# Kernel tuning notes

Hardware: AMD Instinct MI355X
Metric: run time of the kernel (lower is better)

## Reference

```python
import jax, jax.numpy as jnp
import numpy as np

# Module constants (from init_kwargs)
NB_IN = 4          # num_blocks_in
NB_OUT = 8         # num_blocks_out
BS_IN = 128        # block_size_in (hard-coded in source)
NHID = 4096
BS_OUT = NHID // NB_OUT   # 512, also att_out
TOPK = 4
DK = 64            # d_k = d_v, n_head = 1


def _group_linear(x, w):
    # x: (B, n_blocks, d_in), w: (n_blocks, d_in, d_out) -> (B, n_blocks, d_out)
    return jnp.einsum('bnd,nde->bne', x, w)


def _attend(q, k, v):
    # single-head scaled dot-product attention
    attn = jax.nn.softmax(jnp.einsum('bqd,bkd->bqk', q, k) / jnp.sqrt(jnp.asarray(DK, q.dtype)), axis=-1)
    return jnp.einsum('bqk,bkd->bqd', attn, v), attn


def setup_inputs() -> dict:
    key = jax.random.key(0)
    ks = jax.random.split(key, 20)
    s = 0.02
    d = {
        'inp': jax.random.normal(ks[0], (1024, NB_IN * BS_IN), jnp.float32),
        'hx': jax.random.normal(ks[1], (1024, NHID), jnp.float32),
        'cx': jax.random.normal(ks[2], (1024, NHID), jnp.float32),
        # inp_att (residual=False): GroupLinear q/k/v + fc
        'ia_wq': jax.random.normal(ks[3], (NB_OUT, BS_OUT, DK), jnp.float32) * s,
        'ia_wk': jax.random.normal(ks[4], (NB_IN + 1, BS_IN, DK), jnp.float32) * s,
        'ia_wv': jax.random.normal(ks[5], (NB_IN + 1, BS_IN, DK), jnp.float32) * s,
        'ia_fc_w': jax.random.normal(ks[6], (DK, BS_OUT), jnp.float32) * s,
        'ia_fc_b': jnp.zeros((BS_OUT,), jnp.float32),
        # mha (residual=True, gated)
        'mha_wq': jax.random.normal(ks[7], (NB_OUT, BS_OUT, DK), jnp.float32) * s,
        'mha_wk': jax.random.normal(ks[8], (NB_OUT, BS_OUT, DK), jnp.float32) * s,
        'mha_wv': jax.random.normal(ks[9], (NB_OUT, BS_OUT, DK), jnp.float32) * s,
        'mha_fc_w': jax.random.normal(ks[10], (DK, BS_OUT), jnp.float32) * s,
        'mha_fc_b': jnp.zeros((BS_OUT,), jnp.float32),
        'mha_gate_w': jax.random.normal(ks[11], (DK, BS_OUT), jnp.float32) * s,
        'mha_gate_b': jnp.zeros((BS_OUT,), jnp.float32),
        # block-diagonal LSTM (BlockLSTM after blockify_params): per-block LSTMCell
        'w_ih': jax.random.normal(ks[12], (NB_OUT, BS_OUT, 4 * BS_OUT), jnp.float32) * s,
        'w_hh': jax.random.normal(ks[13], (NB_OUT, BS_OUT, 4 * BS_OUT), jnp.float32) * s,
        'b_ih': jnp.zeros((NB_OUT, 4 * BS_OUT), jnp.float32),
        'b_hh': jnp.zeros((NB_OUT, 4 * BS_OUT), jnp.float32),
    }
    return d


def _forward(inp, hx, cx, ia_wq, ia_wk, ia_wv, ia_fc_w, ia_fc_b,
             mha_wq, mha_wk, mha_wv, mha_fc_w, mha_fc_b, mha_gate_w, mha_gate_b,
             w_ih, w_hh, b_ih, b_hh):
    B = inp.shape[0]
    # --- input attention (inp_att) ---
    x = inp.reshape(B, NB_IN, BS_IN)
    x = jnp.concatenate([x, jnp.zeros_like(x[:, :1])], axis=1)        # append null block -> (B, NB_IN+1, BS_IN)
    hb = hx.reshape(B, NB_OUT, BS_OUT)
    q = _group_linear(hb, ia_wq)                                      # (B, NB_OUT, DK)
    k = _group_linear(x, ia_wk)
    v = _group_linear(x, ia_wv)
    o, iatt = _attend(q, k, v)                                        # o:(B,NB_OUT,DK), iatt:(B,NB_OUT,NB_IN+1)
    inp_use = (o @ ia_fc_w + ia_fc_b).reshape(B, NB_OUT * BS_OUT)     # residual=False path

    # --- top-k block selection mask (detached) ---
    score = iatt[:, :, 0]                                             # (B, NB_OUT)
    thr = jax.lax.top_k(score, TOPK)[0][:, -1]                        # k-th largest per sample
    mask_blk = (score > thr[:, None] - 0.01).astype(hx.dtype)         # (B, NB_OUT)
    mask = jnp.broadcast_to(mask_blk[:, :, None], (B, NB_OUT, BS_OUT)).reshape(B, NHID)
    mask = jax.lax.stop_gradient(mask)

    # --- block-diagonal LSTM update ---
    xb = inp_use.reshape(B, NB_OUT, BS_OUT)
    cb = cx.reshape(B, NB_OUT, BS_OUT)
    gates = (jnp.einsum('bkd,kdg->bkg', xb, w_ih) + b_ih
             + jnp.einsum('bkd,kdg->bkg', hb, w_hh) + b_hh)           # (B, NB_OUT, 4*BS_OUT)
    i_g, f_g, g_g, o_g = jnp.split(gates, 4, axis=-1)
    c_new = jax.nn.sigmoid(f_g) * cb + jax.nn.sigmoid(i_g) * jnp.tanh(g_g)
    h_new = jax.nn.sigmoid(o_g) * jnp.tanh(c_new)                     # (B, NB_OUT, BS_OUT)
    cx_new = c_new.reshape(B, NHID)

    # --- inter-block attention (step_att, residual + gate) ---
    residual = h_new
    q2 = _group_linear(h_new, mha_wq)
    k2 = _group_linear(h_new, mha_wk)
    v2 = _group_linear(h_new, mha_wv)
    o2, _ = _attend(q2, k2, v2)                                       # (B, NB_OUT, DK)
    out = o2 @ mha_fc_w + mha_fc_b
    gate = jax.nn.sigmoid(o2 @ mha_gate_w + mha_gate_b)
    hx_new = (residual + gate * jnp.tanh(out)).reshape(B, NHID)

    # --- masked blend of old / new states ---
    hx_out = mask * hx_new + (1.0 - mask) * hx
    cx_out = mask * cx_new + (1.0 - mask) * cx
    return hx_out, cx_out, mask


def reference(inp, hx, cx, ia_wq, ia_wk, ia_wv, ia_fc_w, ia_fc_b,
              mha_wq, mha_wk, mha_wv, mha_fc_w, mha_fc_b, mha_gate_w, mha_gate_b,
              w_ih, w_hh, b_ih, b_hh):
    return _forward(inp, hx, cx, ia_wq, ia_wk, ia_wv, ia_fc_w, ia_fc_b,
                    mha_wq, mha_wk, mha_wv, mha_fc_w, mha_fc_b, mha_gate_w, mha_gate_b,
                    w_ih, w_hh, b_ih, b_hh)
```

## Files before the change

### kernel.cpp

```cpp
#include <hip/hip_runtime.h>
#include <hip/hip_bf16.h>

#define B_    1024
#define NHID_ 4096
#define NBO   8
#define BSO   512
#define DK_   64

typedef __bf16 bf16;
typedef __bf16 bf16x2 __attribute__((ext_vector_type(2)));
typedef __bf16 bf16x4 __attribute__((ext_vector_type(4)));
typedef __bf16 bf16x8 __attribute__((ext_vector_type(8)));
typedef float  f32x4  __attribute__((ext_vector_type(4)));

__device__ __forceinline__ float sigf(float x){ return 1.0f/(1.0f + __expf(-x)); }

__device__ __forceinline__ void gload16(const void* g, void* lds){
    __builtin_amdgcn_global_load_lds((const __attribute__((address_space(1))) unsigned int*)g,
                                     (__attribute__((address_space(3))) unsigned int*)lds,
                                     16, 0, 0);
}

__global__ __launch_bounds__(256) void k_prep(
    const float* __restrict__ hx,
    const float* __restrict__ mha_wq, const float* __restrict__ mha_wk,
    const float* __restrict__ mha_wv, const float* __restrict__ ia_fc_w,
    const float* __restrict__ fc_w, const float* __restrict__ gate_w,
    bf16* __restrict__ hb16, bf16* __restrict__ wqkvT,
    bf16* __restrict__ iafcT, bf16* __restrict__ fcgT)
{
    int gid = blockIdx.x*256 + threadIdx.x;
    if (gid < 1048576){
        float4 v = ((const float4*)hx)[gid];
        bf16x4 o; o.x=(bf16)v.x; o.y=(bf16)v.y; o.z=(bf16)v.z; o.w=(bf16)v.w;
        *(bf16x4*)&hb16[(size_t)gid*4] = o;
        return;
    }
    int e = gid - 1048576;
    if (e < 786432){
        int col = e >> 9, k = e & 511;
        int n = col / 192, c = col - n*192;
        int p = c >> 6, ee = c & 63;
        const float* s = (p==0) ? mha_wq : ((p==1) ? mha_wk : mha_wv);
        wqkvT[e] = (bf16)s[((size_t)n*512 + k)*64 + ee];
        return;
    }
    e -= 786432;
    if (e < 32768){
        int c = e>>6, k = e&63;
        iafcT[e] = (bf16)ia_fc_w[(size_t)k*512 + c];
        return;
    }
    e -= 32768;
    if (e < 65536){
        int cg = e>>6, k = e&63;
        int ct = cg>>6, j = cg&63;
        const float* s = (j<32) ? fc_w : gate_w;
        int col = ct*32 + (j&31);
        fcgT[e] = (bf16)s[(size_t)k*512 + col];
    }
}

__global__ __launch_bounds__(256) void k_wtrans(const float* __restrict__ w_ih,
                                                const float* __restrict__ w_hh,
                                                bf16* __restrict__ wT)
{
    int n = blockIdx.z >> 1, which = blockIdx.z & 1;
    int k0 = blockIdx.y * 64, c0 = blockIdx.x * 64;
    const float* src = (which ? w_hh : w_ih) + (size_t)n*512*2048;
    __shared__ float tile[64][65];
    int t = threadIdx.x;
    #pragma unroll
    for (int it=0; it<4; ++it){
        int idx = t + it*256;
        int r = idx>>4, c4 = (idx&15)*4;
        *(float4*)&tile[r][c4] = *(const float4*)&src[(size_t)(k0+r)*2048 + c0 + c4];
    }
    __syncthreads();
    #pragma unroll
    for (int it=0; it<2; ++it){
        int idx = t + it*256;
        int c = idx>>3, r8 = (idx&7)*8;
        bf16x8 v;
        #pragma unroll
        for (int jj=0;jj<8;++jj) v[jj] = (bf16)tile[r8+jj][c];
        *(bf16x8*)&wT[((size_t)n*2048 + c0 + c)*1024 + which*512 + k0 + r8] = v;
    }
}

__global__ __launch_bounds__(256) void k_qkv(const float* __restrict__ hx,
                                             const float* __restrict__ inp,
                                             const float* __restrict__ ia_wq,
                                             const float* __restrict__ ia_wk,
                                             const float* __restrict__ ia_wv,
                                             float* __restrict__ qbuf,
                                             float* __restrict__ kbuf,
                                             float* __restrict__ vbuf)
{
    int b0 = blockIdx.x*64, y = blockIdx.y, t = threadIdx.x;
    int tx = t&15, ty = t>>4;
    __shared__ float A_s[64][20];
    __shared__ float W1_s[16][68];
    __shared__ float W2_s[16][68];
    if (y < 8){
        int n = y;
        float acc[4][4] = {};
        for (int k0=0; k0<512; k0+=16){
            { int row=t>>2, seg=(t&3)*4;
              *(float4*)&A_s[row][seg] = *(const float4*)&hx[(size_t)(b0+row)*4096 + n*512 + k0 + seg]; }
            { int kk=t>>4, e4=(t&15)*4;
              *(float4*)&W1_s[kk][e4] = *(const float4*)&ia_wq[(size_t)n*32768 + (size_t)(k0+kk)*64 + e4]; }
            __syncthreads();
            #pragma unroll
            for (int kk=0; kk<16; ++kk){
                float4 wv = *(float4*)&W1_s[kk][tx*4];
                #pragma unroll
                for (int r=0;r<4;++r){
                    float a = A_s[ty*4+r][kk];
                    acc[r][0]+=a*wv.x; acc[r][1]+=a*wv.y; acc[r][2]+=a*wv.z; acc[r][3]+=a*wv.w;
                }
            }
            __syncthreads();
        }
        #pragma unroll
        for (int r=0;r<4;++r){
            float4 o; o.x=acc[r][0]; o.y=acc[r][1]; o.z=acc[r][2]; o.w=acc[r][3];
            *(float4*)&qbuf[(size_t)(b0+ty*4+r)*512 + n*64 + tx*4] = o;
        }
    } else {
        int j = y-8;
        float ak[4][4] = {}, av[4][4] = {};
        for (int k0=0; k0<128; k0+=16){
            { int row=t>>2, seg=(t&3)*4;
              *(float4*)&A_s[row][seg] = *(const float4*)&inp[(size_t)(b0+row)*512 + j*128 + k0 + seg]; }
            { int kk=t>>4, e4=(t&15)*4;
              *(float4*)&W1_s[kk][e4] = *(const float4*)&ia_wk[(size_t)j*8192 + (size_t)(k0+kk)*64 + e4];
              *(float4*)&W2_s[kk][e4] = *(const float4*)&ia_wv[(size_t)j*8192 + (size_t)(k0+kk)*64 + e4]; }
            __syncthreads();
            #pragma unroll
            for (int kk=0; kk<16; ++kk){
                float4 wk = *(float4*)&W1_s[kk][tx*4];
                float4 wv = *(float4*)&W2_s[kk][tx*4];
                #pragma unroll
                for (int r=0;r<4;++r){
                    float a = A_s[ty*4+r][kk];
                    ak[r][0]+=a*wk.x; ak[r][1]+=a*wk.y; ak[r][2]+=a*wk.z; ak[r][3]+=a*wk.w;
                    av[r][0]+=a*wv.x; av[r][1]+=a*wv.y; av[r][2]+=a*wv.z; av[r][3]+=a*wv.w;
                }
            }
            __syncthreads();
        }
        #pragma unroll
        for (int r=0;r<4;++r){
            float4 ok; ok.x=ak[r][0]; ok.y=ak[r][1]; ok.z=ak[r][2]; ok.w=ak[r][3];
            float4 ov; ov.x=av[r][0]; ov.y=av[r][1]; ov.z=av[r][2]; ov.w=av[r][3];
            *(float4*)&kbuf[(size_t)(b0+ty*4+r)*256 + j*64 + tx*4] = ok;
            *(float4*)&vbuf[(size_t)(b0+ty*4+r)*256 + j*64 + tx*4] = ov;
        }
    }
}

__global__ __launch_bounds__(256) void k_score(const float* __restrict__ qbuf,
                                               const float* __restrict__ kbuf,
                                               const float* __restrict__ vbuf,
                                               bf16* __restrict__ obuf,
                                               float* __restrict__ maskb,
                                               float* __restrict__ mask_out)
{
    int t = threadIdx.x, sb = t>>6, ts = t&63;
    int b = blockIdx.x*4 + sb;
    __shared__ float q_s[4][512];
    __shared__ float k_s[4][256];
    __shared__ float v_s[4][256];
    __shared__ float at_s[4][40];
    __shared__ float sc_s[4][8];
    __shared__ float mb_s[4][8];

    #pragma unroll
    for (int r=0;r<8;++r) q_s[sb][ts+r*64] = qbuf[(size_t)b*512 + ts + r*64];
    #pragma unroll
    for (int r=0;r<4;++r){
        k_s[sb][ts+r*64] = kbuf[(size_t)b*256 + ts + r*64];
        v_s[sb][ts+r*64] = vbuf[(size_t)b*256 + ts + r*64];
    }
    __syncthreads();
    if (ts < 40){
        int n = ts/5, j = ts%5;
        float s = 0.f;
        if (j < 4){
            const float* q = &q_s[sb][n*64];
            const float* k = &k_s[sb][j*64];
            for (int e=0;e<64;++e) s += q[e]*k[e];
            s *= 0.125f;
        }
        at_s[sb][ts] = s;
    }
    __syncthreads();
    if (ts < 8){
        float m = at_s[sb][ts*5];
        for (int j=1;j<5;++j) m = fmaxf(m, at_s[sb][ts*5+j]);
        float ex[5]; float sum=0.f;
        for (int j=0;j<5;++j){ ex[j]=__expf(at_s[sb][ts*5+j]-m); sum+=ex[j]; }
        float inv = 1.f/sum;
        for (int j=0;j<5;++j) at_s[sb][ts*5+j] = ex[j]*inv;
        sc_s[sb][ts] = ex[0]*inv;
    }
    __syncthreads();
    if (ts == 0){
        float s[8];
        for (int nn=0;nn<8;++nn) s[nn] = sc_s[sb][nn];
        for (int ii=1;ii<8;++ii){ float key=s[ii]; int jj=ii-1;
            while(jj>=0 && s[jj]<key){ s[jj+1]=s[jj]; --jj; } s[jj+1]=key; }
        float thr = s[3]-0.01f;
        for (int nn=0;nn<8;++nn) mb_s[sb][nn] = (sc_s[sb][nn] > thr) ? 1.0f : 0.0f;
    }
    __syncthreads();
    #pragma unroll
    for (int r=0;r<8;++r){
        int i = ts + r*64;
        int n = i>>6, e = i&63;
        float s = 0.f;
        #pragma unroll
        for (int j=0;j<4;++j) s += at_s[sb][n*5+j]*v_s[sb][j*64+e];
        obuf[(size_t)b*512 + i] = (bf16)s;
    }
    if (ts < 8) maskb[b*8+ts] = mb_s[sb][ts];
    float4* mo = (float4*)(mask_out + (size_t)b*4096);
    #pragma unroll
    for (int r=0;r<16;++r){
        int i4 = ts + r*64;
        float m = mb_s[sb][i4>>7];
        float4 mv; mv.x=m; mv.y=m; mv.z=m; mv.w=m;
        mo[i4] = mv;
    }
}

__global__ __launch_bounds__(256) void k_fc_ia(const bf16* __restrict__ obuf,
                                               const bf16* __restrict__ iafcT,
                                               const float* __restrict__ ia_fc_b,
                                               bf16* __restrict__ xb16)
{
    int bx = blockIdx.x, by = blockIdx.y;
    int t = threadIdx.x, w = t>>6, l = t&63, quad = l>>4, l16 = l&15;
    int wm = w&1, wd = w>>1;
    __shared__ bf16 A_s[64*72];
    __shared__ bf16 W_s[64*72];
    #pragma unroll
    for (int j=0;j<2;++j){
        int c = t + j*256;
        int row = c>>3, seg = c&7;
        *(bf16x8*)&A_s[row*72 + seg*8] = *(const bf16x8*)&obuf[((size_t)bx*64+row)*64 + seg*8];
        *(bf16x8*)&W_s[row*72 + seg*8] = *(const bf16x8*)&iafcT[((size_t)by*64+row)*64 + seg*8];
    }
    __syncthreads();
    f32x4 zero = {0.f,0.f,0.f,0.f};
    f32x4 acc[2][2] = {{zero,zero},{zero,zero}};
    #pragma unroll
    for (int k0=0;k0<64;k0+=32){
        bf16x8 a[2], bb[2];
        #pragma unroll
        for (int r=0;r<2;++r) a[r] = *(const bf16x8*)&A_s[(wm*32+r*16+l16)*72 + k0 + quad*8];
        #pragma unroll
        for (int c=0;c<2;++c) bb[c] = *(const bf16x8*)&W_s[(wd*32+c*16+l16)*72 + k0 + quad*8];
        #pragma unroll
        for (int r=0;r<2;++r)
            #pragma unroll
            for (int c=0;c<2;++c)
                acc[r][c] = __builtin_amdgcn_mfma_f32_16x16x32_bf16(a[r], bb[c], acc[r][c], 0,0,0);
    }
    #pragma unroll
    for (int c=0;c<2;++c){
        int col = by*64 + wd*32 + c*16 + l16;
        float bias = ia_fc_b[col];
        #pragma unroll
        for (int r=0;r<2;++r)
            #pragma unroll
            for (int v=0;v<4;++v){
                int row = bx*64 + wm*32 + r*16 + quad*4 + v;
                xb16[(size_t)row*512 + col] = (bf16)(acc[r][c][v] + bias);
            }
    }
}

__global__ __launch_bounds__(256,4) void k_lstm(
    const bf16* __restrict__ xb16, const bf16* __restrict__ hb16,
    const bf16* __restrict__ wT, const float* __restrict__ b_ih,
    const float* __restrict__ b_hh, const float* __restrict__ cx,
    const float* __restrict__ maskb,
    float* __restrict__ cx_out, bf16* __restrict__ hn16)
{
    int bid = blockIdx.x;
    int n = bid & 7;
    int i = bid >> 3;
    int d0 = (i & 15) * 32;
    int b0 = (i >> 4) * 128;
    int t = threadIdx.x;
    int w = t >> 6, l = t & 63;
    int quad = l >> 4, l16 = l & 15;
    int wm = w & 1, wd = w >> 1;

    __shared__ bf16 A_s[512*8];
    __shared__ bf16 W_s[512*8];

    f32x4 zero = {0.f,0.f,0.f,0.f};
    f32x4 acc[4][4];
    #pragma unroll
    for (int rf=0;rf<4;++rf)
        #pragma unroll
        for (int g=0;g<4;++g) acc[rf][g] = zero;

    const bf16* wbase = wT + (size_t)n*2048*1024;

    for (int k0 = 0; k0 < 1024; k0 += 32){
        const bf16* ab = (k0 < 512) ? (xb16 + (size_t)n*512 + k0)
                                    : (hb16 + (size_t)n*512 + (k0-512));
        #pragma unroll
        for (int j=0;j<2;++j){
            int slot = j*256 + w*64 + l;
            int row = slot>>2, ss = slot&3;
            int seg = ss ^ ((row>>1)&3);
            gload16(ab + (size_t)(b0+row)*4096 + seg*8, &A_s[(size_t)(j*256 + w*64)*8]);
        }
        #pragma unroll
        for (int j=0;j<2;++j){
            int slot = j*256 + w*64 + l;
            int col = slot>>2, ss = slot&3;
            int seg = ss ^ ((col>>1)&3);
            int g = col>>5, dl = col&31;
            gload16(wbase + (size_t)(g*512 + d0 + dl)*1024 + k0 + seg*8,
                    &W_s[(size_t)(j*256 + w*64)*8]);
        }
        __syncthreads();
        bf16x8 a[4];
        #pragma unroll
        for (int rf=0;rf<4;++rf){
            int row = wm*64 + rf*16 + l16;
            int slot = row*4 + (quad ^ ((row>>1)&3));
            a[rf] = *(const bf16x8*)&A_s[slot*8];
        }
        #pragma unroll
        for (int g=0; g<4; ++g){
            int col = g*32 + wd*16 + l16;
            int slot = col*4 + (quad ^ ((col>>1)&3));
            bf16x8 bb = *(const bf16x8*)&W_s[slot*8];
            #pragma unroll
            for (int rf=0;rf<4;++rf)
                acc[rf][g] = __builtin_amdgcn_mfma_f32_16x16x32_bf16(a[rf], bb, acc[rf][g], 0,0,0);
        }
        __syncthreads();
    }

    int d = d0 + wd*16 + l16;
    float bi  = b_ih[n*2048 +        d] + b_hh[n*2048 +        d];
    float bff = b_ih[n*2048 +  512 + d] + b_hh[n*2048 +  512 + d];
    float bg  = b_ih[n*2048 + 1024 + d] + b_hh[n*2048 + 1024 + d];
    float bo  = b_ih[n*2048 + 1536 + d] + b_hh[n*2048 + 1536 + d];
    #pragma unroll
    for (int rf=0;rf<4;++rf){
        #pragma unroll
        for (int v=0;v<4;++v){
            int row = b0 + wm*64 + rf*16 + quad*4 + v;
            float gi = acc[rf][0][v] + bi;
            float gf = acc[rf][1][v] + bff;
            float gg = acc[rf][2][v] + bg;
            float go = acc[rf][3][v] + bo;
            size_t gidx = (size_t)row*4096 + n*512 + d;
            float cb = cx[gidx];
            float cn = sigf(gf)*cb + sigf(gi)*tanhf(gg);
            float hn = sigf(go)*tanhf(cn);
            float m  = maskb[row*8+n];
            cx_out[gidx] = (m != 0.f) ? cn : cb;
            hn16[gidx]   = (bf16)hn;
        }
    }
}

__global__ __launch_bounds__(256) void k_proj64(const bf16* __restrict__ hn16,
                                                const bf16* __restrict__ wqkvT,
                                                float* __restrict__ qkv2)
{
    int b0 = blockIdx.x*64, n = blockIdx.y, ct = blockIdx.z;
    int t = threadIdx.x, w = t>>6, l = t&63, quad = l>>4, l16 = l&15;
    int wm = w&1, wd = w>>1;
    __shared__ bf16 A_s[256*8];
    __shared__ bf16 B_s[256*8];
    f32x4 zero = {0.f,0.f,0.f,0.f};
    f32x4 acc[2][2] = {{zero,zero},{zero,zero}};
    const bf16* ab = hn16 + (size_t)n*512;
    const bf16* wb = wqkvT + ((size_t)n*192 + ct*64)*512;

    for (int k0=0;k0<512;k0+=32){
        {
            int slot = t;
            int row = slot>>2, ss = slot&3;
            int seg = ss ^ ((row>>1)&3);
            gload16(ab + (size_t)(b0+row)*4096 + k0 + seg*8, &A_s[(size_t)(w*64)*8]);
            gload16(wb + (size_t)row*512      + k0 + seg*8, &B_s[(size_t)(w*64)*8]);
        }
        __syncthreads();
        bf16x8 a[2], bb[2];
        #pragma unroll
        for (int r=0;r<2;++r){
            int row = wm*32 + r*16 + l16;
            int slot = row*4 + (quad ^ ((row>>1)&3));
            a[r] = *(const bf16x8*)&A_s[slot*8];
        }
        #pragma unroll
        for (int c=0;c<2;++c){
            int col = wd*32 + c*16 + l16;
            int slot = col*4 + (quad ^ ((col>>1)&3));
            bb[c] = *(const bf16x8*)&B_s[slot*8];
        }
        #pragma unroll
        for (int r=0;r<2;++r)
            #pragma unroll
            for (int c=0;c<2;++c)
                acc[r][c] = __builtin_amdgcn_mfma_f32_16x16x32_bf16(a[r], bb[c], acc[r][c], 0,0,0);
        __syncthreads();
    }
    #pragma unroll
    for (int c=0;c<2;++c){
        int col = ct*64 + wd*32 + c*16 + l16;
        #pragma unroll
        for (int r=0;r<2;++r)
            #pragma unroll
            for (int v=0;v<4;++v){
                int row = b0 + wm*32 + r*16 + quad*4 + v;
                qkv2[(size_t)row*1536 + n*192 + col] = acc[r][c][v];
            }
    }
}

__global__ __launch_bounds__(256) void k_att2(const float* __restrict__ qkv2,
                                              bf16* __restrict__ o2buf)
{
    int t = threadIdx.x, sb = t>>6, ts = t&63;
    int b = blockIdx.x*4 + sb;
    __shared__ float q_s[4][512];
    __shared__ float k_s[4][512];
    __shared__ float v_s[4][512];
    __shared__ float at_s[4][64];
    #pragma unroll
    for (int r=0;r<8;++r){
        int i = ts + r*64;
        int n = i>>6, e = i&63;
        const float* src = qkv2 + (size_t)b*1536 + n*192;
        q_s[sb][i] = src[e];
        k_s[sb][i] = src[64+e];
        v_s[sb][i] = src[128+e];
    }
    __syncthreads();
    {
        int n = ts>>3, j = ts&7;
        float s = 0.f;
        const float* q = &q_s[sb][n*64];
        const float* k = &k_s[sb][j*64];
        for (int e=0;e<64;++e) s += q[e]*k[e];
        at_s[sb][ts] = s*0.125f;
    }
    __syncthreads();
    if (ts < 8){
        float m = at_s[sb][ts*8];
        for (int j=1;j<8;++j) m = fmaxf(m, at_s[sb][ts*8+j]);
        float ex[8]; float sum=0.f;
        for (int j=0;j<8;++j){ ex[j]=__expf(at_s[sb][ts*8+j]-m); sum+=ex[j]; }
        float inv = 1.f/sum;
        for (int j=0;j<8;++j) at_s[sb][ts*8+j] = ex[j]*inv;
    }
    __syncthreads();
    #pragma unroll
    for (int r=0;r<8;++r){
        int i = ts + r*64;
        int n = i>>6, e = i&63;
        float s = 0.f;
        #pragma unroll
        for (int j=0;j<8;++j) s += at_s[sb][n*8+j]*v_s[sb][j*64+e];
        o2buf[(size_t)b*512 + i] = (bf16)s;
    }
}

__global__ __launch_bounds__(256) void k_fcgate(const bf16* __restrict__ o2buf,
                                                const bf16* __restrict__ fcgT,
                                                const float* __restrict__ fc_b,
                                                const float* __restrict__ gate_b,
                                                const bf16* __restrict__ hn16,
                                                const float* __restrict__ hx,
                                                const float* __restrict__ maskb,
                                                float* __restrict__ hx_out)
{
    int bx = blockIdx.x, ct = blockIdx.y;
    int t = threadIdx.x, w = t>>6, l = t&63, quad = l>>4, l16 = l&15;
    __shared__ bf16 A_s[64*72];
    __shared__ bf16 W_s[64*72];
    #pragma unroll
    for (int j=0;j<2;++j){
        int c = t + j*256;
        int row = c>>3, seg = c&7;
        *(bf16x8*)&A_s[row*72 + seg*8] = *(const bf16x8*)&o2buf[((size_t)bx*64+row)*64 + seg*8];
        *(bf16x8*)&W_s[row*72 + seg*8] = *(const bf16x8*)&fcgT[((size_t)ct*64+row)*64 + seg*8];
    }
    __syncthreads();
    f32x4 zero = {0.f,0.f,0.f,0.f};
    f32x4 acc[4] = {zero,zero,zero,zero};
    #pragma unroll
    for (int k0=0;k0<64;k0+=32){
        bf16x8 a = *(const bf16x8*)&A_s[(w*16+l16)*72 + k0 + quad*8];
        #pragma unroll
        for (int c=0;c<4;++c){
            bf16x8 bb = *(const bf16x8*)&W_s[(c*16+l16)*72 + k0 + quad*8];
            acc[c] = __builtin_amdgcn_mfma_f32_16x16x32_bf16(a, bb, acc[c], 0,0,0);
        }
    }
    #pragma unroll
    for (int c=0;c<2;++c){
        int d = ct*32 + c*16 + l16;
        float fb = fc_b[d], gb = gate_b[d];
        #pragma unroll
        for (int v=0;v<4;++v){
            int row = bx*64 + w*16 + quad*4 + v;
            int b = row>>3, n = row&7;
            size_t idx = (size_t)b*4096 + n*512 + d;
            float f = acc[c][v]   + fb;
            float g = acc[c+2][v] + gb;
            float hn = (float)hn16[idx];
            float m = maskb[row];
            hx_out[idx] = (m != 0.f) ? (hn + sigf(g)*tanhf(f)) : hx[idx];
        }
    }
}

extern "C" void kernel_launch(void* const* d_in, const int* in_sizes, int n_in,
                              void* d_out, int out_size, void* d_ws, size_t ws_size,
                              hipStream_t stream)
{
    const float* inp       = (const float*)d_in[0];
    const float* hx        = (const float*)d_in[1];
    const float* cx        = (const float*)d_in[2];
    const float* ia_wq     = (const float*)d_in[3];
    const float* ia_wk     = (const float*)d_in[4];
    const float* ia_wv     = (const float*)d_in[5];
    const float* ia_fc_w   = (const float*)d_in[6];
    const float* ia_fc_b   = (const float*)d_in[7];
    const float* mha_wq    = (const float*)d_in[8];
    const float* mha_wk    = (const float*)d_in[9];
    const float* mha_wv    = (const float*)d_in[10];
    const float* mha_fc_w  = (const float*)d_in[11];
    const float* mha_fc_b  = (const float*)d_in[12];
    const float* mha_gate_w= (const float*)d_in[13];
    const float* mha_gate_b= (const float*)d_in[14];
    const float* w_ih      = (const float*)d_in[15];
    const float* w_hh      = (const float*)d_in[16];
    const float* b_ih      = (const float*)d_in[17];
    const float* b_hh      = (const float*)d_in[18];

    float* hx_out  = (float*)d_out;
    float* cx_out  = hx_out + (size_t)B_*NHID_;
    float* mask_out= cx_out + (size_t)B_*NHID_;

    char* p = (char*)d_ws;
    bf16* wT     = (bf16*)p;               p += (size_t)8*2048*1024*2;
    bf16* hb16   = (bf16*)p;               p += (size_t)B_*NHID_*2;
    bf16* xb16   = (bf16*)p;               p += (size_t)B_*NHID_*2;
    bf16* hn16   = (bf16*)p;               p += (size_t)B_*NHID_*2;
    bf16* wqkvT  = (bf16*)p;               p += (size_t)8*192*512*2;
    bf16* iafcT  = (bf16*)p;               p += (size_t)512*64*2;
    bf16* fcgT   = (bf16*)p;               p += (size_t)1024*64*2;
    float* qbuf  = (float*)p;              p += (size_t)B_*512*4;
    float* kbuf  = (float*)p;              p += (size_t)B_*256*4;
    float* vbuf  = (float*)p;              p += (size_t)B_*256*4;
    bf16* obuf   = (bf16*)p;               p += (size_t)B_*8*64*2;
    bf16* o2buf  = (bf16*)p;               p += (size_t)B_*8*64*2;
    float* qkv2  = (float*)p;              p += (size_t)B_*1536*4;
    float* maskb = (float*)p;              p += (size_t)B_*8*4;

    hipLaunchKernelGGL(k_prep, dim3(7552), dim3(256), 0, stream,
                       hx, mha_wq, mha_wk, mha_wv, ia_fc_w, mha_fc_w, mha_gate_w,
                       hb16, wqkvT, iafcT, fcgT);
    hipLaunchKernelGGL(k_wtrans, dim3(32,8,16), dim3(256), 0, stream, w_ih, w_hh, wT);
    hipLaunchKernelGGL(k_qkv, dim3(16,12), dim3(256), 0, stream,
                       hx, inp, ia_wq, ia_wk, ia_wv, qbuf, kbuf, vbuf);
    hipLaunchKernelGGL(k_score, dim3(256), dim3(256), 0, stream,
                       qbuf, kbuf, vbuf, obuf, maskb, mask_out);
    hipLaunchKernelGGL(k_fc_ia, dim3(128,8), dim3(256), 0, stream, obuf, iafcT, ia_fc_b, xb16);
    hipLaunchKernelGGL(k_lstm, dim3(1024), dim3(256), 0, stream,
                       xb16, hb16, wT, b_ih, b_hh, cx, maskb, cx_out, hn16);
    hipLaunchKernelGGL(k_proj64, dim3(16,8,3), dim3(256), 0, stream, hn16, wqkvT, qkv2);
    hipLaunchKernelGGL(k_att2, dim3(256), dim3(256), 0, stream, qkv2, o2buf);
    hipLaunchKernelGGL(k_fcgate, dim3(128,16), dim3(256), 0, stream,
                       o2buf, fcgT, mha_fc_b, mha_gate_b, hn16, hx, maskb, hx_out);
}
```

Baseline: 317.7 us.

## Double-buffer LSTM and proj GEMMs, merge weight transpose into prep, retile qkv

Several independent changes ship together. The LSTM and proj64 GEMMs now double-buffer their LDS tiles, so the next K-slice's global_load_lds is issued before the current slice's MFMAs and one barrier per iteration is dropped. The w_ih/w_hh transpose kernel is folded into k_prep to save a launch. k_qkv uses 32-row tiles with a K step of 32 for more blocks, k_fcgate processes two column tiles per block, and sigmoid/tanh use a fast rcp-based approximation. These add LDS pressure and may cost a little accuracy in tanh.

```diff
diff --git a/kernel.cpp b/kernel.cpp
--- a/kernel.cpp
+++ b/kernel.cpp
@@ -13,7 +13,14 @@
 typedef __bf16 bf16x8 __attribute__((ext_vector_type(8)));
 typedef float  f32x4  __attribute__((ext_vector_type(4)));
 
-__device__ __forceinline__ float sigf(float x){ return 1.0f/(1.0f + __expf(-x)); }
+__device__ __forceinline__ float sigf(float x){
+    float e = __expf(-x);
+    return __builtin_amdgcn_rcpf(1.0f + e);
+}
+__device__ __forceinline__ float ftanh(float x){
+    float e = __expf(2.0f*x);
+    return 1.0f - 2.0f*__builtin_amdgcn_rcpf(e + 1.0f);
+}
 
 __device__ __forceinline__ void gload16(const void* g, void* lds){
     __builtin_amdgcn_global_load_lds((const __attribute__((address_space(1))) unsigned int*)g,
@@ -22,14 +29,42 @@
 }
 
 __global__ __launch_bounds__(256) void k_prep(
+    const float* __restrict__ w_ih, const float* __restrict__ w_hh,
     const float* __restrict__ hx,
     const float* __restrict__ mha_wq, const float* __restrict__ mha_wk,
     const float* __restrict__ mha_wv, const float* __restrict__ ia_fc_w,
     const float* __restrict__ fc_w, const float* __restrict__ gate_w,
-    bf16* __restrict__ hb16, bf16* __restrict__ wqkvT,
+    bf16* __restrict__ wT, bf16* __restrict__ hb16, bf16* __restrict__ wqkvT,
     bf16* __restrict__ iafcT, bf16* __restrict__ fcgT)
 {
-    int gid = blockIdx.x*256 + threadIdx.x;
+    int bid = blockIdx.x;
+    int t = threadIdx.x;
+    if (bid < 4096){
+        int c0 = (bid & 31)*64;
+        int k0 = ((bid>>5)&7)*64;
+        int z  = bid>>8;
+        int n = z>>1, which = z&1;
+        const float* src = (which ? w_hh : w_ih) + (size_t)n*512*2048;
+        __shared__ float tile[64][65];
+        #pragma unroll
+        for (int it=0; it<4; ++it){
+            int idx = t + it*256;
+            int r = idx>>4, c4 = (idx&15)*4;
+            *(float4*)&tile[r][c4] = *(const float4*)&src[(size_t)(k0+r)*2048 + c0 + c4];
+        }
+        __syncthreads();
+        #pragma unroll
+        for (int it=0; it<2; ++it){
+            int idx = t + it*256;
+            int c = idx>>3, r8 = (idx&7)*8;
+            bf16x8 v;
+            #pragma unroll
+            for (int jj=0;jj<8;++jj) v[jj] = (bf16)tile[r8+jj][c];
+            *(bf16x8*)&wT[((size_t)n*2048 + c0 + c)*1024 + which*512 + k0 + r8] = v;
+        }
+        return;
+    }
+    int gid = (bid-4096)*256 + t;
     if (gid < 1048576){
         float4 v = ((const float4*)hx)[gid];
         bf16x4 o; o.x=(bf16)v.x; o.y=(bf16)v.y; o.z=(bf16)v.z; o.w=(bf16)v.w;
@@ -61,33 +96,6 @@
     }
 }
 
-__global__ __launch_bounds__(256) void k_wtrans(const float* __restrict__ w_ih,
-                                                const float* __restrict__ w_hh,
-                                                bf16* __restrict__ wT)
-{
-    int n = blockIdx.z >> 1, which = blockIdx.z & 1;
-    int k0 = blockIdx.y * 64, c0 = blockIdx.x * 64;
-    const float* src = (which ? w_hh : w_ih) + (size_t)n*512*2048;
-    __shared__ float tile[64][65];
-    int t = threadIdx.x;
-    #pragma unroll
-    for (int it=0; it<4; ++it){
-        int idx = t + it*256;
-        int r = idx>>4, c4 = (idx&15)*4;
-        *(float4*)&tile[r][c4] = *(const float4*)&src[(size_t)(k0+r)*2048 + c0 + c4];
-    }
-    __syncthreads();
-    #pragma unroll
-    for (int it=0; it<2; ++it){
-        int idx = t + it*256;
-        int c = idx>>3, r8 = (idx&7)*8;
-        bf16x8 v;
-        #pragma unroll
-        for (int jj=0;jj<8;++jj) v[jj] = (bf16)tile[r8+jj][c];
-        *(bf16x8*)&wT[((size_t)n*2048 + c0 + c)*1024 + which*512 + k0 + r8] = v;
-    }
-}
-
 __global__ __launch_bounds__(256) void k_qkv(const float* __restrict__ hx,
                                              const float* __restrict__ inp,
                                              const float* __restrict__ ia_wq,
@@ -97,65 +105,82 @@
                                              float* __restrict__ kbuf,
                                              float* __restrict__ vbuf)
 {
-    int b0 = blockIdx.x*64, y = blockIdx.y, t = threadIdx.x;
+    int b0 = blockIdx.x*32, y = blockIdx.y, t = threadIdx.x;
     int tx = t&15, ty = t>>4;
-    __shared__ float A_s[64][20];
-    __shared__ float W1_s[16][68];
-    __shared__ float W2_s[16][68];
+    __shared__ float Af[32][36];
+    __shared__ float W1[32][68];
+    __shared__ float W2[32][68];
     if (y < 8){
         int n = y;
-        float acc[4][4] = {};
-        for (int k0=0; k0<512; k0+=16){
-            { int row=t>>2, seg=(t&3)*4;
-              *(float4*)&A_s[row][seg] = *(const float4*)&hx[(size_t)(b0+row)*4096 + n*512 + k0 + seg]; }
-            { int kk=t>>4, e4=(t&15)*4;
-              *(float4*)&W1_s[kk][e4] = *(const float4*)&ia_wq[(size_t)n*32768 + (size_t)(k0+kk)*64 + e4]; }
+        float acc[2][4] = {};
+        for (int k0=0; k0<512; k0+=32){
+            { int row=t>>3, c4=(t&7)*4;
+              *(float4*)&Af[row][c4] = *(const float4*)&hx[(size_t)(b0+row)*4096 + n*512 + k0 + c4]; }
+            #pragma unroll
+            for (int j=0;j<2;++j){
+                int id = j*256 + t;
+                int kk = id>>4, e4 = (id&15)*4;
+                *(float4*)&W1[kk][e4] = *(const float4*)&ia_wq[(size_t)n*32768 + (size_t)(k0+kk)*64 + e4];
+            }
             __syncthreads();
             #pragma unroll
-            for (int kk=0; kk<16; ++kk){
-                float4 wv = *(float4*)&W1_s[kk][tx*4];
+            for (int kk4=0; kk4<8; ++kk4){
+                float4 a0 = *(float4*)&Af[ty*2  ][kk4*4];
+                float4 a1 = *(float4*)&Af[ty*2+1][kk4*4];
                 #pragma unroll
-                for (int r=0;r<4;++r){
-                    float a = A_s[ty*4+r][kk];
-                    acc[r][0]+=a*wv.x; acc[r][1]+=a*wv.y; acc[r][2]+=a*wv.z; acc[r][3]+=a*wv.w;
+                for (int j=0;j<4;++j){
+                    float4 wv = *(float4*)&W1[kk4*4+j][tx*4];
+                    float s0 = (j==0)?a0.x:((j==1)?a0.y:((j==2)?a0.z:a0.w));
+                    float s1 = (j==0)?a1.x:((j==1)?a1.y:((j==2)?a1.z:a1.w));
+                    acc[0][0]+=s0*wv.x; acc[0][1]+=s0*wv.y; acc[0][2]+=s0*wv.z; acc[0][3]+=s0*wv.w;
+                    acc[1][0]+=s1*wv.x; acc[1][1]+=s1*wv.y; acc[1][2]+=s1*wv.z; acc[1][3]+=s1*wv.w;
                 }
             }
             __syncthreads();
         }
         #pragma unroll
-        for (int r=0;r<4;++r){
+        for (int r=0;r<2;++r){
             float4 o; o.x=acc[r][0]; o.y=acc[r][1]; o.z=acc[r][2]; o.w=acc[r][3];
-            *(float4*)&qbuf[(size_t)(b0+ty*4+r)*512 + n*64 + tx*4] = o;
+            *(float4*)&qbuf[(size_t)(b0+ty*2+r)*512 + n*64 + tx*4] = o;
         }
     } else {
-        int j = y-8;
-        float ak[4][4] = {}, av[4][4] = {};
-        for (int k0=0; k0<128; k0+=16){
-            { int row=t>>2, seg=(t&3)*4;
-              *(float4*)&A_s[row][seg] = *(const float4*)&inp[(size_t)(b0+row)*512 + j*128 + k0 + seg]; }
-            { int kk=t>>4, e4=(t&15)*4;
-              *(float4*)&W1_s[kk][e4] = *(const float4*)&ia_wk[(size_t)j*8192 + (size_t)(k0+kk)*64 + e4];
-              *(float4*)&W2_s[kk][e4] = *(const float4*)&ia_wv[(size_t)j*8192 + (size_t)(k0+kk)*64 + e4]; }
+        int jb = y-8;
+        float ak[2][4] = {}, av[2][4] = {};
+        for (int k0=0; k0<128; k0+=32){
+            { int row=t>>3, c4=(t&7)*4;
+              *(float4*)&Af[row][c4] = *(const float4*)&inp[(size_t)(b0+row)*512 + jb*128 + k0 + c4]; }
+            #pragma unroll
+            for (int j=0;j<2;++j){
+                int id = j*256 + t;
+                int kk = id>>4, e4 = (id&15)*4;
+                *(float4*)&W1[kk][e4] = *(const float4*)&ia_wk[(size_t)jb*8192 + (size_t)(k0+kk)*64 + e4];
+                *(float4*)&W2[kk][e4] = *(const float4*)&ia_wv[(size_t)jb*8192 + (size_t)(k0+kk)*64 + e4];
+            }
             __syncthreads();
             #pragma unroll
-            for (int kk=0; kk<16; ++kk){
-                float4 wk = *(float4*)&W1_s[kk][tx*4];
-                float4 wv = *(float4*)&W2_s[kk][tx*4];
+            for (int kk4=0; kk4<8; ++kk4){
+                float4 a0 = *(float4*)&Af[ty*2  ][kk4*4];
+                float4 a1 = *(float4*)&Af[ty*2+1][kk4*4];
                 #pragma unroll
-                for (int r=0;r<4;++r){
-                    float a = A_s[ty*4+r][kk];
-                    ak[r][0]+=a*wk.x; ak[r][1]+=a*wk.y; ak[r][2]+=a*wk.z; ak[r][3]+=a*wk.w;
-                    av[r][0]+=a*wv.x; av[r][1]+=a*wv.y; av[r][2]+=a*wv.z; av[r][3]+=a*wv.w;
+                for (int j=0;j<4;++j){
+                    float4 wk = *(float4*)&W1[kk4*4+j][tx*4];
+                    float4 wv = *(float4*)&W2[kk4*4+j][tx*4];
+                    float s0 = (j==0)?a0.x:((j==1)?a0.y:((j==2)?a0.z:a0.w));
+                    float s1 = (j==0)?a1.x:((j==1)?a1.y:((j==2)?a1.z:a1.w));
+                    ak[0][0]+=s0*wk.x; ak[0][1]+=s0*wk.y; ak[0][2]+=s0*wk.z; ak[0][3]+=s0*wk.w;
+                    ak[1][0]+=s1*wk.x; ak[1][1]+=s1*wk.y; ak[1][2]+=s1*wk.z; ak[1][3]+=s1*wk.w;
+                    av[0][0]+=s0*wv.x; av[0][1]+=s0*wv.y; av[0][2]+=s0*wv.z; av[0][3]+=s0*wv.w;
+                    av[1][0]+=s1*wv.x; av[1][1]+=s1*wv.y; av[1][2]+=s1*wv.z; av[1][3]+=s1*wv.w;
                 }
             }
             __syncthreads();
         }
         #pragma unroll
-        for (int r=0;r<4;++r){
+        for (int r=0;r<2;++r){
             float4 ok; ok.x=ak[r][0]; ok.y=ak[r][1]; ok.z=ak[r][2]; ok.w=ak[r][3];
             float4 ov; ov.x=av[r][0]; ov.y=av[r][1]; ov.z=av[r][2]; ov.w=av[r][3];
-            *(float4*)&kbuf[(size_t)(b0+ty*4+r)*256 + j*64 + tx*4] = ok;
-            *(float4*)&vbuf[(size_t)(b0+ty*4+r)*256 + j*64 + tx*4] = ov;
+            *(float4*)&kbuf[(size_t)(b0+ty*2+r)*256 + jb*64 + tx*4] = ok;
+            *(float4*)&vbuf[(size_t)(b0+ty*2+r)*256 + jb*64 + tx*4] = ov;
         }
     }
 }
@@ -299,8 +324,8 @@
     int quad = l >> 4, l16 = l & 15;
     int wm = w & 1, wd = w >> 1;
 
-    __shared__ bf16 A_s[512*8];
-    __shared__ bf16 W_s[512*8];
+    __shared__ bf16 A_s[2][512*8];
+    __shared__ bf16 W_s[2][512*8];
 
     f32x4 zero = {0.f,0.f,0.f,0.f};
     f32x4 acc[4][4];
@@ -311,7 +336,7 @@
 
     const bf16* wbase = wT + (size_t)n*2048*1024;
 
-    for (int k0 = 0; k0 < 1024; k0 += 32){
+    auto stage = [&](int buf, int k0){
         const bf16* ab = (k0 < 512) ? (xb16 + (size_t)n*512 + k0)
                                     : (hb16 + (size_t)n*512 + (k0-512));
         #pragma unroll
@@ -319,7 +344,7 @@
             int slot = j*256 + w*64 + l;
             int row = slot>>2, ss = slot&3;
             int seg = ss ^ ((row>>1)&3);
-            gload16(ab + (size_t)(b0+row)*4096 + seg*8, &A_s[(size_t)(j*256 + w*64)*8]);
+            gload16(ab + (size_t)(b0+row)*4096 + seg*8, &A_s[buf][(j*256 + w*64)*8]);
         }
         #pragma unroll
         for (int j=0;j<2;++j){
@@ -328,26 +353,31 @@
             int seg = ss ^ ((col>>1)&3);
             int g = col>>5, dl = col&31;
             gload16(wbase + (size_t)(g*512 + d0 + dl)*1024 + k0 + seg*8,
-                    &W_s[(size_t)(j*256 + w*64)*8]);
-        }
+                    &W_s[buf][(j*256 + w*64)*8]);
+        }
+    };
+
+    stage(0, 0);
+    for (int it = 0; it < 32; ++it){
         __syncthreads();
+        if (it < 31) stage((it+1)&1, (it+1)*32);
+        int buf = it & 1;
         bf16x8 a[4];
         #pragma unroll
         for (int rf=0;rf<4;++rf){
             int row = wm*64 + rf*16 + l16;
             int slot = row*4 + (quad ^ ((row>>1)&3));
-            a[rf] = *(const bf16x8*)&A_s[slot*8];
+            a[rf] = *(const bf16x8*)&A_s[buf][slot*8];
         }
         #pragma unroll
         for (int g=0; g<4; ++g){
             int col = g*32 + wd*16 + l16;
             int slot = col*4 + (quad ^ ((col>>1)&3));
-            bf16x8 bb = *(const bf16x8*)&W_s[slot*8];
+            bf16x8 bb = *(const bf16x8*)&W_s[buf][slot*8];
             #pragma unroll
             for (int rf=0;rf<4;++rf)
                 acc[rf][g] = __builtin_amdgcn_mfma_f32_16x16x32_bf16(a[rf], bb, acc[rf][g], 0,0,0);
         }
-        __syncthreads();
     }
 
     int d = d0 + wd*16 + l16;
@@ -366,8 +396,8 @@
             float go = acc[rf][3][v] + bo;
             size_t gidx = (size_t)row*4096 + n*512 + d;
             float cb = cx[gidx];
-            float cn = sigf(gf)*cb + sigf(gi)*tanhf(gg);
-            float hn = sigf(go)*tanhf(cn);
+            float cn = sigf(gf)*cb + sigf(gi)*ftanh(gg);
+            float hn = sigf(go)*ftanh(cn);
             float m  = maskb[row*8+n];
             cx_out[gidx] = (m != 0.f) ? cn : cb;
             hn16[gidx]   = (bf16)hn;
@@ -382,41 +412,43 @@
     int b0 = blockIdx.x*64, n = blockIdx.y, ct = blockIdx.z;
     int t = threadIdx.x, w = t>>6, l = t&63, quad = l>>4, l16 = l&15;
     int wm = w&1, wd = w>>1;
-    __shared__ bf16 A_s[256*8];
-    __shared__ bf16 B_s[256*8];
+    __shared__ bf16 A_s[2][256*8];
+    __shared__ bf16 B_s[2][256*8];
     f32x4 zero = {0.f,0.f,0.f,0.f};
     f32x4 acc[2][2] = {{zero,zero},{zero,zero}};
     const bf16* ab = hn16 + (size_t)n*512;
     const bf16* wb = wqkvT + ((size_t)n*192 + ct*64)*512;
 
-    for (int k0=0;k0<512;k0+=32){
-        {
-            int slot = t;
-            int row = slot>>2, ss = slot&3;
-            int seg = ss ^ ((row>>1)&3);
-            gload16(ab + (size_t)(b0+row)*4096 + k0 + seg*8, &A_s[(size_t)(w*64)*8]);
-            gload16(wb + (size_t)row*512      + k0 + seg*8, &B_s[(size_t)(w*64)*8]);
-        }
+    auto stage = [&](int buf, int k0){
+        int row = t>>2, ss = t&3;
+        int seg = ss ^ ((row>>1)&3);
+        gload16(ab + (size_t)(b0+row)*4096 + k0 + seg*8, &A_s[buf][(w*64)*8]);
+        gload16(wb + (size_t)row*512      + k0 + seg*8, &B_s[buf][(w*64)*8]);
+    };
+
+    stage(0, 0);
+    for (int it=0; it<16; ++it){
         __syncthreads();
+        if (it < 15) stage((it+1)&1, (it+1)*32);
+        int buf = it&1;
         bf16x8 a[2], bb[2];
         #pragma unroll
         for (int r=0;r<2;++r){
             int row = wm*32 + r*16 + l16;
             int slot = row*4 + (quad ^ ((row>>1)&3));
-            a[r] = *(const bf16x8*)&A_s[slot*8];
+            a[r] = *(const bf16x8*)&A_s[buf][slot*8];
         }
         #pragma unroll
         for (int c=0;c<2;++c){
             int col = wd*32 + c*16 + l16;
             int slot = col*4 + (quad ^ ((col>>1)&3));
-            bb[c] = *(const bf16x8*)&B_s[slot*8];
+            bb[c] = *(const bf16x8*)&B_s[buf][slot*8];
         }
         #pragma unroll
         for (int r=0;r<2;++r)
             #pragma unroll
             for (int c=0;c<2;++c)
                 acc[r][c] = __builtin_amdgcn_mfma_f32_16x16x32_bf16(a[r], bb[c], acc[r][c], 0,0,0);
-        __syncthreads();
     }
     #pragma unroll
     for (int c=0;c<2;++c){
@@ -488,43 +520,48 @@
                                                 const float* __restrict__ maskb,
                                                 float* __restrict__ hx_out)
 {
-    int bx = blockIdx.x, ct = blockIdx.y;
+    int bx = blockIdx.x, ct0 = blockIdx.y*2;
     int t = threadIdx.x, w = t>>6, l = t&63, quad = l>>4, l16 = l&15;
     __shared__ bf16 A_s[64*72];
-    __shared__ bf16 W_s[64*72];
+    __shared__ bf16 W_s[2][64*72];
     #pragma unroll
     for (int j=0;j<2;++j){
         int c = t + j*256;
         int row = c>>3, seg = c&7;
         *(bf16x8*)&A_s[row*72 + seg*8] = *(const bf16x8*)&o2buf[((size_t)bx*64+row)*64 + seg*8];
-        *(bf16x8*)&W_s[row*72 + seg*8] = *(const bf16x8*)&fcgT[((size_t)ct*64+row)*64 + seg*8];
+        *(bf16x8*)&W_s[0][row*72 + seg*8] = *(const bf16x8*)&fcgT[((size_t)ct0*64+row)*64 + seg*8];
+        *(bf16x8*)&W_s[1][row*72 + seg*8] = *(const bf16x8*)&fcgT[((size_t)(ct0+1)*64+row)*64 + seg*8];
     }
     __syncthreads();
     f32x4 zero = {0.f,0.f,0.f,0.f};
-    f32x4 acc[4] = {zero,zero,zero,zero};
-    #pragma unroll
-    for (int k0=0;k0<64;k0+=32){
-        bf16x8 a = *(const bf16x8*)&A_s[(w*16+l16)*72 + k0 + quad*8];
-        #pragma unroll
-        for (int c=0;c<4;++c){
-            bf16x8 bb = *(const bf16x8*)&W_s[(c*16+l16)*72 + k0 + quad*8];
-            acc[c] = __builtin_amdgcn_mfma_f32_16x16x32_bf16(a, bb, acc[c], 0,0,0);
-        }
-    }
-    #pragma unroll
-    for (int c=0;c<2;++c){
-        int d = ct*32 + c*16 + l16;
-        float fb = fc_b[d], gb = gate_b[d];
-        #pragma unroll
-        for (int v=0;v<4;++v){
-            int row = bx*64 + w*16 + quad*4 + v;
-            int b = row>>3, n = row&7;
-            size_t idx = (size_t)b*4096 + n*512 + d;
-            float f = acc[c][v]   + fb;
-            float g = acc[c+2][v] + gb;
-            float hn = (float)hn16[idx];
-            float m = maskb[row];
-            hx_out[idx] = (m != 0.f) ? (hn + sigf(g)*tanhf(f)) : hx[idx];
+    #pragma unroll
+    for (int cc=0; cc<2; ++cc){
+        int ct = ct0 + cc;
+        f32x4 acc[4] = {zero,zero,zero,zero};
+        #pragma unroll
+        for (int k0=0;k0<64;k0+=32){
+            bf16x8 a = *(const bf16x8*)&A_s[(w*16+l16)*72 + k0 + quad*8];
+            #pragma unroll
+            for (int c=0;c<4;++c){
+                bf16x8 bb = *(const bf16x8*)&W_s[cc][(c*16+l16)*72 + k0 + quad*8];
+                acc[c] = __builtin_amdgcn_mfma_f32_16x16x32_bf16(a, bb, acc[c], 0,0,0);
+            }
+        }
+        #pragma unroll
+        for (int c=0;c<2;++c){
+            int d = ct*32 + c*16 + l16;
+            float fb = fc_b[d], gb = gate_b[d];
+            #pragma unroll
+            for (int v=0;v<4;++v){
+                int row = bx*64 + w*16 + quad*4 + v;
+                int b = row>>3, n = row&7;
+                size_t idx = (size_t)b*4096 + n*512 + d;
+                float f = acc[c][v]   + fb;
+                float g = acc[c+2][v] + gb;
+                float hn = (float)hn16[idx];
+                float m = maskb[row];
+                hx_out[idx] = (m != 0.f) ? (hn + sigf(g)*ftanh(f)) : hx[idx];
+            }
         }
     }
 }
@@ -573,11 +610,10 @@
     float* qkv2  = (float*)p;              p += (size_t)B_*1536*4;
     float* maskb = (float*)p;              p += (size_t)B_*8*4;
 
-    hipLaunchKernelGGL(k_prep, dim3(7552), dim3(256), 0, stream,
-                       hx, mha_wq, mha_wk, mha_wv, ia_fc_w, mha_fc_w, mha_gate_w,
-                       hb16, wqkvT, iafcT, fcgT);
-    hipLaunchKernelGGL(k_wtrans, dim3(32,8,16), dim3(256), 0, stream, w_ih, w_hh, wT);
-    hipLaunchKernelGGL(k_qkv, dim3(16,12), dim3(256), 0, stream,
+    hipLaunchKernelGGL(k_prep, dim3(11648), dim3(256), 0, stream,
+                       w_ih, w_hh, hx, mha_wq, mha_wk, mha_wv, ia_fc_w, mha_fc_w, mha_gate_w,
+                       wT, hb16, wqkvT, iafcT, fcgT);
+    hipLaunchKernelGGL(k_qkv, dim3(32,12), dim3(256), 0, stream,
                        hx, inp, ia_wq, ia_wk, ia_wv, qbuf, kbuf, vbuf);
     hipLaunchKernelGGL(k_score, dim3(256), dim3(256), 0, stream,
                        qbuf, kbuf, vbuf, obuf, maskb, mask_out);
@@ -586,6 +622,6 @@
                        xb16, hb16, wT, b_ih, b_hh, cx, maskb, cx_out, hn16);
     hipLaunchKernelGGL(k_proj64, dim3(16,8,3), dim3(256), 0, stream, hn16, wqkvT, qkv2);
     hipLaunchKernelGGL(k_att2, dim3(256), dim3(256), 0, stream, qkv2, o2buf);
-    hipLaunchKernelGGL(k_fcgate, dim3(128,16), dim3(256), 0, stream,
+    hipLaunchKernelGGL(k_fcgate, dim3(128,8), dim3(256), 0, stream,
                        o2buf, fcgT, mha_fc_b, mha_gate_b, hn16, hx, maskb, hx_out);
 }
```

Result: faster. 287.6 us (-9.5%).
